# Performance work log

Measured on AMD Instinct MI355X. Metric: run time of the kernel, lower is better.

## Reference

```python
import jax, jax.numpy as jnp
import numpy as np

B, N, CQ, CH, H = 4, 1024, 512, 512, 8
D = CH // H  # head_dim = 64


def setup_inputs() -> dict:
    key = jax.random.key(0)
    ks = jax.random.split(key, 8)
    s = jnp.float32(0.02)  # realistic (non-degenerate) init scale instead of the module's zeros
    return {
        "q_x": jax.random.normal(ks[0], (B, N, CQ), jnp.float32),
        "attn_bias": jax.random.normal(ks[1], (B, H, N, N), jnp.float32),
        "Wq": jax.random.normal(ks[2], (CH, CQ), jnp.float32) * s,
        "bq": jnp.zeros((CH,), jnp.float32),
        "Wk": jax.random.normal(ks[3], (CH, CQ), jnp.float32) * s,  # LinearNoBias
        "Wv": jax.random.normal(ks[4], (CH, CQ), jnp.float32) * s,  # LinearNoBias
        "Wo": jax.random.normal(ks[5], (CQ, CH), jnp.float32) * s,
        "bo": jnp.zeros((CQ,), jnp.float32),
        "Wg": jax.random.normal(ks[6], (CQ, CQ), jnp.float32) * s,
        "bg": jnp.zeros((CQ,), jnp.float32),
        "gating_bias": jnp.ones((CQ,), jnp.float32),
    }


def reference(q_x, attn_bias, Wq, bq, Wk, Wv, Wo, bo, Wg, bg, gating_bias):
    Bq, Nq, _ = q_x.shape
    scale = jnp.asarray(D, q_x.dtype) ** -0.5
    # QKV projections; self-attention path (q_x is kv_x, ndim==3) applies scale to q
    q = (q_x @ Wq.T + bq).reshape(Bq, Nq, H, D).transpose(0, 2, 1, 3) * scale  # [B,H,N,D]
    k = (q_x @ Wk.T).reshape(Bq, Nq, H, D).transpose(0, 2, 1, 3)               # [B,H,N,D]
    v = (q_x @ Wv.T).reshape(Bq, Nq, H, D).transpose(0, 2, 1, 3)               # [B,H,N,D]
    # bias-augmented attention
    logits = jnp.einsum("bhqd,bhkd->bhqk", q, k) + attn_bias                    # [B,H,N,N]
    a = jax.nn.softmax(logits, axis=-1)
    o = jnp.einsum("bhqk,bhkd->bhqd", a, v)                                     # [B,H,N,D]
    o = o.transpose(0, 2, 1, 3).reshape(Bq, Nq, CH)                             # flatten heads
    out = o @ Wo.T + bo                                                         # to_out: c_hidden -> c_q
    # sigmoid gating with learned gating_bias (init ones)
    gate = jax.nn.sigmoid(q_x @ Wg.T + bg + gating_bias)
    return out * gate
```

## Files before the change

kernel.cpp:

```cpp
#include <hip/hip_runtime.h>
#include <math.h>


typedef __bf16 bf16x8 __attribute__((ext_vector_type(8)));
typedef float f32x4 __attribute__((ext_vector_type(4)));

__device__ __forceinline__ unsigned short f2bf(float f) {
    union { float f; unsigned u; } v; v.f = f;
    unsigned r = v.u + 0x7fff + ((v.u >> 16) & 1);
    return (unsigned short)(r >> 16);
}

__device__ __forceinline__ bf16x8 ldb8(const unsigned short* p) {
    union { float4 f; bf16x8 b; } u;
    u.f = *(const float4*)p;
    return u.b;
}

__global__ __launch_bounds__(256) void convert_kernel(
    const float* __restrict__ X, const float* __restrict__ Wq,
    const float* __restrict__ Wk, const float* __restrict__ Wg,
    const float* __restrict__ Wv, const float* __restrict__ Wo,
    unsigned short* __restrict__ Xb, unsigned short* __restrict__ Wcat)
{
    int i4 = (blockIdx.x * 256 + threadIdx.x) * 4;
    const float* src;
    unsigned short* dst;
    int off;
    if (i4 < 2097152) {
        src = X; dst = Xb; off = i4;
    } else {
        int g = i4 - 2097152;
        int sect = g >> 18;
        src = (sect == 0) ? Wq : (sect == 1) ? Wk : (sect == 2) ? Wg
            : (sect == 3) ? Wv : Wo;
        dst = Wcat + (sect << 18);
        off = g & 262143;
    }
    float4 v = *(const float4*)&src[off];
    ushort4 u;
    u.x = f2bf(v.x); u.y = f2bf(v.y); u.z = f2bf(v.z); u.w = f2bf(v.w);
    *(ushort4*)&dst[off] = u;
}

#define GSTR 40

__device__ __forceinline__ void gemm_core(
    const unsigned short* __restrict__ Ag,
    const unsigned short* __restrict__ Bg,
    unsigned short* __restrict__ Ab, unsigned short* __restrict__ Bb,
    f32x4 acc[4][4])
{
    const int tid = threadIdx.x;
    const int lane = tid & 63;
    const int quad = lane >> 4, lx = lane & 15;
    const int wid = tid >> 6;
    const int mw0 = (wid >> 1) * 64, nw0 = (wid & 1) * 64;
    const int rA = tid >> 2, cA = (tid & 3) * 8;
    const int l0 = rA * GSTR + cA;
    const int l1 = (rA + 64) * GSTR + cA;

    float4 a0 = *(const float4*)&Ag[(size_t)rA * 512 + cA];
    float4 a1 = *(const float4*)&Ag[(size_t)(rA + 64) * 512 + cA];
    float4 b0 = *(const float4*)&Bg[(size_t)rA * 512 + cA];
    float4 b1 = *(const float4*)&Bg[(size_t)(rA + 64) * 512 + cA];

#pragma unroll 1
    for (int k0 = 0; k0 < 512; k0 += 32) {
        *(float4*)&Ab[l0] = a0;
        *(float4*)&Ab[l1] = a1;
        *(float4*)&Bb[l0] = b0;
        *(float4*)&Bb[l1] = b1;
        __syncthreads();
        if (k0 < 480) {
            int kn = k0 + 32;
            a0 = *(const float4*)&Ag[(size_t)rA * 512 + kn + cA];
            a1 = *(const float4*)&Ag[(size_t)(rA + 64) * 512 + kn + cA];
            b0 = *(const float4*)&Bg[(size_t)rA * 512 + kn + cA];
            b1 = *(const float4*)&Bg[(size_t)(rA + 64) * 512 + kn + cA];
        }
        bf16x8 af[4], bfr[4];
#pragma unroll
        for (int mi = 0; mi < 4; ++mi)
            af[mi] = ldb8(&Ab[(mw0 + mi * 16 + lx) * GSTR + quad * 8]);
#pragma unroll
        for (int ni = 0; ni < 4; ++ni)
            bfr[ni] = ldb8(&Bb[(nw0 + ni * 16 + lx) * GSTR + quad * 8]);
#pragma unroll
        for (int mi = 0; mi < 4; ++mi)
#pragma unroll
            for (int ni = 0; ni < 4; ++ni)
                acc[mi][ni] = __builtin_amdgcn_mfma_f32_16x16x32_bf16(
                    af[mi], bfr[ni], acc[mi][ni], 0, 0, 0);
        __syncthreads();
    }
}

__global__ __launch_bounds__(256) void proj_gemm(
    const unsigned short* __restrict__ Xb, const unsigned short* __restrict__ Wcat,
    const float* __restrict__ bq, const float* __restrict__ bg,
    const float* __restrict__ gbias,
    unsigned short* __restrict__ qb, unsigned short* __restrict__ kb,
    unsigned short* __restrict__ vtb, float* __restrict__ gateb)
{
    __shared__ __align__(16) unsigned short Ab[128 * GSTR];
    __shared__ __align__(16) unsigned short Bb[128 * GSTR];
    const int row0 = blockIdx.x * 128;
    const int colv0 = blockIdx.y * 128;
    f32x4 acc[4][4];
#pragma unroll
    for (int i = 0; i < 4; ++i)
#pragma unroll
        for (int j = 0; j < 4; ++j) acc[i][j] = (f32x4){0.f, 0.f, 0.f, 0.f};

    gemm_core(Xb + (size_t)row0 * 512, Wcat + (size_t)colv0 * 512, Ab, Bb, acc);

    const int tid = threadIdx.x;
    const int lane = tid & 63;
    const int quad = lane >> 4, lx = lane & 15;
    const int wid = tid >> 6;
    const int mw0 = (wid >> 1) * 64, nw0 = (wid & 1) * 64;
    const int wsel = colv0 >> 9;
    const int ncb = colv0 & 511;

    if (wsel == 0) {
#pragma unroll
        for (int mi = 0; mi < 4; ++mi) {
#pragma unroll
            for (int ni = 0; ni < 4; ++ni) {
                int ch = ncb + nw0 + ni * 16 + lx;
                int h = ch >> 6, d = ch & 63;
                float bias = bq[ch];
#pragma unroll
                for (int r = 0; r < 4; ++r) {
                    int m = row0 + mw0 + mi * 16 + quad * 4 + r;
                    int b = m >> 10, nn = m & 1023;
                    qb[(size_t)(b * 8 + h) * 65536 + (size_t)nn * 64 + d] =
                        f2bf((acc[mi][ni][r] + bias) * 0.125f);
                }
            }
        }
    } else if (wsel == 1) {
#pragma unroll
        for (int mi = 0; mi < 4; ++mi) {
#pragma unroll
            for (int ni = 0; ni < 4; ++ni) {
                int ch = ncb + nw0 + ni * 16 + lx;
                int h = ch >> 6, d = ch & 63;
#pragma unroll
                for (int r = 0; r < 4; ++r) {
                    int m = row0 + mw0 + mi * 16 + quad * 4 + r;
                    int b = m >> 10, nn = m & 1023;
                    kb[(size_t)(b * 8 + h) * 65536 + (size_t)nn * 64 + d] =
                        f2bf(acc[mi][ni][r]);
                }
            }
        }
    } else if (wsel == 2) {
#pragma unroll
        for (int mi = 0; mi < 4; ++mi) {
#pragma unroll
            for (int ni = 0; ni < 4; ++ni) {
                int ch = ncb + nw0 + ni * 16 + lx;
                float bias = bg[ch] + gbias[ch];
#pragma unroll
                for (int r = 0; r < 4; ++r) {
                    int m = row0 + mw0 + mi * 16 + quad * 4 + r;
                    float z = acc[mi][ni][r] + bias;
                    gateb[(size_t)m * 512 + ch] = 1.f / (1.f + __expf(-z));
                }
            }
        }
    } else {
#pragma unroll
        for (int mi = 0; mi < 4; ++mi) {
            int tok0 = row0 + mw0 + mi * 16 + quad * 4;
            int b = tok0 >> 10, nn0 = tok0 & 1023;
#pragma unroll
            for (int ni = 0; ni < 4; ++ni) {
                int ch = ncb + nw0 + ni * 16 + lx;
                int h = ch >> 6, d = ch & 63;
                ushort4 u;
                u.x = f2bf(acc[mi][ni][0]);
                u.y = f2bf(acc[mi][ni][1]);
                u.z = f2bf(acc[mi][ni][2]);
                u.w = f2bf(acc[mi][ni][3]);
                *(ushort4*)&vtb[(size_t)(b * 8 + h) * 65536 + (size_t)d * 1024 + nn0] = u;
            }
        }
    }
}

#define LSTR 72

__global__ __launch_bounds__(256) void attn_kernel(
    const unsigned short* __restrict__ qb, const unsigned short* __restrict__ kb,
    const unsigned short* __restrict__ vtb, const float* __restrict__ bias,
    unsigned short* __restrict__ obb)
{
    __shared__ unsigned short QPs[64 * LSTR];
    __shared__ unsigned short Ks[64 * LSTR];
    __shared__ unsigned short Vt[64 * LSTR];

    const int tid = threadIdx.x;
    const int bh = blockIdx.y;
    const int qr0 = blockIdx.x * 64;
    const int wv = tid >> 6, lane = tid & 63;
    const int quad = lane >> 4, lx = lane & 15;
    const int qw0 = wv * 16;

    const unsigned short* qp = qb + (size_t)bh * 65536;
    const unsigned short* kp = kb + (size_t)bh * 65536;
    const unsigned short* vp = vtb + (size_t)bh * 65536;
    const float* bp = bias + (size_t)bh * 1048576;

    const int sr0 = tid >> 3, sc0 = (tid & 7) * 8;
    const int sr1 = (tid + 256) >> 3, sc1 = (tid & 7) * 8;

    *(float4*)&QPs[sr0 * LSTR + sc0] = *(const float4*)&qp[(size_t)(qr0 + sr0) * 64 + sc0];
    *(float4*)&QPs[sr1 * LSTR + sc1] = *(const float4*)&qp[(size_t)(qr0 + sr1) * 64 + sc1];

    float4 kr0 = *(const float4*)&kp[(size_t)sr0 * 64 + sc0];
    float4 kr1 = *(const float4*)&kp[(size_t)sr1 * 64 + sc1];
    float4 vr0 = *(const float4*)&vp[(size_t)sr0 * 1024 + sc0];
    float4 vr1 = *(const float4*)&vp[(size_t)sr1 * 1024 + sc1];

    const float* bbase = bp + (size_t)(qr0 + qw0 + quad * 4) * 1024 + lx;
    float bv[4][4];
#pragma unroll
    for (int r = 0; r < 4; ++r)
#pragma unroll
        for (int c = 0; c < 4; ++c)
            bv[r][c] = bbase[(size_t)r * 1024 + c * 16];

    __syncthreads();

    bf16x8 aq0 = ldb8(&QPs[(qw0 + lx) * LSTR + quad * 8]);
    bf16x8 aq1 = ldb8(&QPs[(qw0 + lx) * LSTR + 32 + quad * 8]);

    float l_i[4] = {0.f, 0.f, 0.f, 0.f};
    f32x4 oacc[4];
#pragma unroll
    for (int c = 0; c < 4; ++c) oacc[c] = (f32x4){0.f, 0.f, 0.f, 0.f};

#pragma unroll 1
    for (int kt = 0; kt < 16; ++kt) {
        __syncthreads();
        *(float4*)&Ks[sr0 * LSTR + sc0] = kr0;
        *(float4*)&Ks[sr1 * LSTR + sc1] = kr1;
        *(float4*)&Vt[sr0 * LSTR + sc0] = vr0;
        *(float4*)&Vt[sr1 * LSTR + sc1] = vr1;
        __syncthreads();

        const int ktn = (kt + 1) & 15;
        kr0 = *(const float4*)&kp[(size_t)(ktn * 64 + sr0) * 64 + sc0];
        kr1 = *(const float4*)&kp[(size_t)(ktn * 64 + sr1) * 64 + sc1];
        vr0 = *(const float4*)&vp[(size_t)sr0 * 1024 + ktn * 64 + sc0];
        vr1 = *(const float4*)&vp[(size_t)sr1 * 1024 + ktn * 64 + sc1];
        float bvn[4][4];
#pragma unroll
        for (int r = 0; r < 4; ++r)
#pragma unroll
            for (int c = 0; c < 4; ++c)
                bvn[r][c] = bbase[(size_t)r * 1024 + ktn * 64 + c * 16];

        f32x4 sacc[4];
#pragma unroll
        for (int c = 0; c < 4; ++c) {
            bf16x8 bk0 = ldb8(&Ks[(c * 16 + lx) * LSTR + quad * 8]);
            bf16x8 bk1 = ldb8(&Ks[(c * 16 + lx) * LSTR + 32 + quad * 8]);
            f32x4 z = {0.f, 0.f, 0.f, 0.f};
            z = __builtin_amdgcn_mfma_f32_16x16x32_bf16(aq0, bk0, z, 0, 0, 0);
            z = __builtin_amdgcn_mfma_f32_16x16x32_bf16(aq1, bk1, z, 0, 0, 0);
            sacc[c] = z;
        }

#pragma unroll
        for (int r = 0; r < 4; ++r) {
            float p0 = __expf(sacc[0][r] + bv[r][0]);
            float p1 = __expf(sacc[1][r] + bv[r][1]);
            float p2 = __expf(sacc[2][r] + bv[r][2]);
            float p3 = __expf(sacc[3][r] + bv[r][3]);
            l_i[r] += p0 + p1 + p2 + p3;
            int prow = (qw0 + quad * 4 + r) * LSTR;
            QPs[prow + 0 * 16 + lx] = f2bf(p0);
            QPs[prow + 1 * 16 + lx] = f2bf(p1);
            QPs[prow + 2 * 16 + lx] = f2bf(p2);
            QPs[prow + 3 * 16 + lx] = f2bf(p3);
        }

        bf16x8 ap0 = ldb8(&QPs[(qw0 + lx) * LSTR + quad * 8]);
        bf16x8 ap1 = ldb8(&QPs[(qw0 + lx) * LSTR + 32 + quad * 8]);
#pragma unroll
        for (int c = 0; c < 4; ++c) {
            bf16x8 bv0 = ldb8(&Vt[(c * 16 + lx) * LSTR + quad * 8]);
            bf16x8 bv1 = ldb8(&Vt[(c * 16 + lx) * LSTR + 32 + quad * 8]);
            oacc[c] = __builtin_amdgcn_mfma_f32_16x16x32_bf16(ap0, bv0, oacc[c], 0, 0, 0);
            oacc[c] = __builtin_amdgcn_mfma_f32_16x16x32_bf16(ap1, bv1, oacc[c], 0, 0, 0);
        }

#pragma unroll
        for (int r = 0; r < 4; ++r)
#pragma unroll
            for (int c = 0; c < 4; ++c)
                bv[r][c] = bvn[r][c];
    }

    const int b = bh >> 3, h = bh & 7;
#pragma unroll
    for (int r = 0; r < 4; ++r) {
        float lt = l_i[r];
        lt += __shfl_xor(lt, 1);
        lt += __shfl_xor(lt, 2);
        lt += __shfl_xor(lt, 4);
        lt += __shfl_xor(lt, 8);
        float inv = 1.f / lt;
        int row = qr0 + qw0 + quad * 4 + r;
        unsigned short* op = obb + (size_t)(b * 1024 + row) * 512 + h * 64 + lx;
#pragma unroll
        for (int c = 0; c < 4; ++c)
            op[c * 16] = f2bf(oacc[c][r] * inv);
    }
}

__global__ __launch_bounds__(256) void out_gemm(
    const unsigned short* __restrict__ A, const unsigned short* __restrict__ WoB,
    const float* __restrict__ bo, const float* __restrict__ gateb,
    float* __restrict__ out)
{
    __shared__ __align__(16) unsigned short Ab[64 * GSTR];
    __shared__ __align__(16) unsigned short Bb[128 * GSTR];
    const int tid = threadIdx.x;
    const int row0 = blockIdx.x * 64;
    const int n0 = blockIdx.y * 128;
    const unsigned short* Ag = A + (size_t)row0 * 512;
    const unsigned short* Bg = WoB + (size_t)n0 * 512;

    const int lane = tid & 63;
    const int quad = lane >> 4, lx = lane & 15;
    const int wid = tid >> 6;
    const int mw0 = (wid & 1) * 32, nw0 = (wid >> 1) * 64;
    const int rA = tid >> 2, cA = (tid & 3) * 8;
    const int lA = rA * GSTR + cA;
    const int lB0 = lA;
    const int lB1 = (rA + 64) * GSTR + cA;

    f32x4 acc[2][4];
#pragma unroll
    for (int i = 0; i < 2; ++i)
#pragma unroll
        for (int j = 0; j < 4; ++j) acc[i][j] = (f32x4){0.f, 0.f, 0.f, 0.f};

    float4 a0 = *(const float4*)&Ag[(size_t)rA * 512 + cA];
    float4 b0 = *(const float4*)&Bg[(size_t)rA * 512 + cA];
    float4 b1 = *(const float4*)&Bg[(size_t)(rA + 64) * 512 + cA];

#pragma unroll 1
    for (int k0 = 0; k0 < 512; k0 += 32) {
        *(float4*)&Ab[lA] = a0;
        *(float4*)&Bb[lB0] = b0;
        *(float4*)&Bb[lB1] = b1;
        __syncthreads();
        if (k0 < 480) {
            int kn = k0 + 32;
            a0 = *(const float4*)&Ag[(size_t)rA * 512 + kn + cA];
            b0 = *(const float4*)&Bg[(size_t)rA * 512 + kn + cA];
            b1 = *(const float4*)&Bg[(size_t)(rA + 64) * 512 + kn + cA];
        }
        bf16x8 af[2], bfr[4];
#pragma unroll
        for (int mi = 0; mi < 2; ++mi)
            af[mi] = ldb8(&Ab[(mw0 + mi * 16 + lx) * GSTR + quad * 8]);
#pragma unroll
        for (int ni = 0; ni < 4; ++ni)
            bfr[ni] = ldb8(&Bb[(nw0 + ni * 16 + lx) * GSTR + quad * 8]);
#pragma unroll
        for (int mi = 0; mi < 2; ++mi)
#pragma unroll
            for (int ni = 0; ni < 4; ++ni)
                acc[mi][ni] = __builtin_amdgcn_mfma_f32_16x16x32_bf16(
                    af[mi], bfr[ni], acc[mi][ni], 0, 0, 0);
        __syncthreads();
    }

#pragma unroll
    for (int mi = 0; mi < 2; ++mi) {
#pragma unroll
        for (int ni = 0; ni < 4; ++ni) {
            int n = n0 + nw0 + ni * 16 + lx;
            float bias = bo[n];
#pragma unroll
            for (int r = 0; r < 4; ++r) {
                int m = row0 + mw0 + mi * 16 + quad * 4 + r;
                out[(size_t)m * 512 + n] =
                    (acc[mi][ni][r] + bias) * gateb[(size_t)m * 512 + n];
            }
        }
    }
}

extern "C" void kernel_launch(void* const* d_in, const int* in_sizes, int n_in,
                              void* d_out, int out_size, void* d_ws, size_t ws_size,
                              hipStream_t stream) {
    (void)in_sizes; (void)n_in; (void)out_size; (void)ws_size;
    const float* q_x   = (const float*)d_in[0];
    const float* bias  = (const float*)d_in[1];
    const float* Wq    = (const float*)d_in[2];
    const float* bq    = (const float*)d_in[3];
    const float* Wk    = (const float*)d_in[4];
    const float* Wv    = (const float*)d_in[5];
    const float* Wo    = (const float*)d_in[6];
    const float* bo    = (const float*)d_in[7];
    const float* Wg    = (const float*)d_in[8];
    const float* bg    = (const float*)d_in[9];
    const float* gbias = (const float*)d_in[10];
    float* out = (float*)d_out;

    char* ws = (char*)d_ws;
    unsigned short* qb   = (unsigned short*)ws;
    unsigned short* kb   = (unsigned short*)(ws + (4u << 20));
    unsigned short* vtb  = (unsigned short*)(ws + (8u << 20));
    float* gateb         = (float*)(ws + (12u << 20));
    unsigned short* obb  = (unsigned short*)(ws + (20u << 20));
    unsigned short* Xb   = (unsigned short*)(ws + (24u << 20));
    unsigned short* Wcat = (unsigned short*)(ws + (28u << 20));

    convert_kernel<<<3328, 256, 0, stream>>>(q_x, Wq, Wk, Wg, Wv, Wo, Xb, Wcat);
    proj_gemm<<<dim3(32, 16), dim3(256), 0, stream>>>(
        Xb, Wcat, bq, bg, gbias, qb, kb, vtb, gateb);
    attn_kernel<<<dim3(16, 32), dim3(256), 0, stream>>>(qb, kb, vtb, bias, obb);
    out_gemm<<<dim3(64, 4), dim3(256), 0, stream>>>(
        obb, Wcat + (size_t)2048 * 512, bo, gateb, out);
}
```

Before: 266.2 us.

## Fuse all stages into one cooperative persistent kernel with grid syncs

Replaces the four separate launches (convert, projection GEMM, attention, output GEMM) with a single cooperative kernel of 512 blocks that runs each stage in turn, separated by grid-wide barriers. The aim is to remove per-launch overhead and inter-kernel gaps. The out-GEMM stage is re-tiled to 64x64 so it fits the fixed 512-block grid. The risks are grid-sync cost, occupancy limits from requesting two blocks per CU, and load imbalance because every stage is forced onto the same grid size. A fallback to the old multi-kernel path runs when occupancy is insufficient.

New measurement: 266.2 us. About the same (+0.0%).

```diff
diff --git a/kernel.cpp b/kernel.cpp
--- a/kernel.cpp
+++ b/kernel.cpp
@@ -1,5 +1,8 @@
 #include <hip/hip_runtime.h>
+#include <hip/hip_cooperative_groups.h>
 #include <math.h>
+
+namespace cg = cooperative_groups;
 
 
 typedef __bf16 bf16x8 __attribute__((ext_vector_type(8)));
@@ -15,6 +18,357 @@
     union { float4 f; bf16x8 b; } u;
     u.f = *(const float4*)p;
     return u.b;
+}
+
+#define GSTR 40
+#define LSTR 72
+
+__global__ __launch_bounds__(256, 2) void fused_kernel(
+    const float* __restrict__ X, const float* __restrict__ bias,
+    const float* __restrict__ Wq, const float* __restrict__ bq,
+    const float* __restrict__ Wk, const float* __restrict__ Wv,
+    const float* __restrict__ Wo, const float* __restrict__ bo,
+    const float* __restrict__ Wg, const float* __restrict__ bg,
+    const float* __restrict__ gbias, float* __restrict__ out,
+    unsigned short* __restrict__ qb, unsigned short* __restrict__ kb,
+    unsigned short* __restrict__ vtb, float* __restrict__ gateb,
+    unsigned short* __restrict__ obb,
+    unsigned short* __restrict__ Xb, unsigned short* __restrict__ Wcat)
+{
+    cg::grid_group grid = cg::this_grid();
+    __shared__ __align__(16) unsigned short smem[14336];
+
+    const int blk = blockIdx.x;
+    const int tid = threadIdx.x;
+    const int lane = tid & 63;
+    const int quad = lane >> 4, lx = lane & 15;
+    const int wid = tid >> 6;
+
+    {
+        int idx = blk * 256 + tid;
+#pragma unroll 1
+        for (int it = 0; it < 7; ++it) {
+            int chunk = idx + it * 131072;
+            if (chunk < 851968) {
+                int i4 = chunk * 4;
+                const float* src; unsigned short* dst; int off;
+                if (i4 < 2097152) { src = X; dst = Xb; off = i4; }
+                else {
+                    int g = i4 - 2097152;
+                    int sect = g >> 18;
+                    src = (sect == 0) ? Wq : (sect == 1) ? Wk : (sect == 2) ? Wg
+                        : (sect == 3) ? Wv : Wo;
+                    dst = Wcat + (sect << 18);
+                    off = g & 262143;
+                }
+                float4 v = *(const float4*)&src[off];
+                ushort4 u;
+                u.x = f2bf(v.x); u.y = f2bf(v.y); u.z = f2bf(v.z); u.w = f2bf(v.w);
+                *(ushort4*)&dst[off] = u;
+            }
+        }
+    }
+    grid.sync();
+
+    {
+        unsigned short* Ab = smem;
+        unsigned short* Bb = smem + 128 * GSTR;
+        const int row0 = (blk & 31) * 128;
+        const int colv0 = (blk >> 5) * 128;
+        const unsigned short* Ag = Xb + (size_t)row0 * 512;
+        const unsigned short* Bg = Wcat + (size_t)colv0 * 512;
+        const int mw0 = (wid >> 1) * 64, nw0 = (wid & 1) * 64;
+        const int rA = tid >> 2, cA = (tid & 3) * 8;
+        const int l0 = rA * GSTR + cA;
+        const int l1 = (rA + 64) * GSTR + cA;
+
+        f32x4 acc[4][4];
+#pragma unroll
+        for (int i = 0; i < 4; ++i)
+#pragma unroll
+            for (int j = 0; j < 4; ++j) acc[i][j] = (f32x4){0.f, 0.f, 0.f, 0.f};
+
+        float4 a0 = *(const float4*)&Ag[(size_t)rA * 512 + cA];
+        float4 a1 = *(const float4*)&Ag[(size_t)(rA + 64) * 512 + cA];
+        float4 b0 = *(const float4*)&Bg[(size_t)rA * 512 + cA];
+        float4 b1 = *(const float4*)&Bg[(size_t)(rA + 64) * 512 + cA];
+
+#pragma unroll 1
+        for (int k0 = 0; k0 < 512; k0 += 32) {
+            *(float4*)&Ab[l0] = a0;
+            *(float4*)&Ab[l1] = a1;
+            *(float4*)&Bb[l0] = b0;
+            *(float4*)&Bb[l1] = b1;
+            __syncthreads();
+            if (k0 < 480) {
+                int kn = k0 + 32;
+                a0 = *(const float4*)&Ag[(size_t)rA * 512 + kn + cA];
+                a1 = *(const float4*)&Ag[(size_t)(rA + 64) * 512 + kn + cA];
+                b0 = *(const float4*)&Bg[(size_t)rA * 512 + kn + cA];
+                b1 = *(const float4*)&Bg[(size_t)(rA + 64) * 512 + kn + cA];
+            }
+            bf16x8 af[4], bfr[4];
+#pragma unroll
+            for (int mi = 0; mi < 4; ++mi)
+                af[mi] = ldb8(&Ab[(mw0 + mi * 16 + lx) * GSTR + quad * 8]);
+#pragma unroll
+            for (int ni = 0; ni < 4; ++ni)
+                bfr[ni] = ldb8(&Bb[(nw0 + ni * 16 + lx) * GSTR + quad * 8]);
+#pragma unroll
+            for (int mi = 0; mi < 4; ++mi)
+#pragma unroll
+                for (int ni = 0; ni < 4; ++ni)
+                    acc[mi][ni] = __builtin_amdgcn_mfma_f32_16x16x32_bf16(
+                        af[mi], bfr[ni], acc[mi][ni], 0, 0, 0);
+            __syncthreads();
+        }
+
+        const int wsel = colv0 >> 9;
+        const int ncb = colv0 & 511;
+        if (wsel == 0) {
+#pragma unroll
+            for (int mi = 0; mi < 4; ++mi) {
+#pragma unroll
+                for (int ni = 0; ni < 4; ++ni) {
+                    int ch = ncb + nw0 + ni * 16 + lx;
+                    int h = ch >> 6, d = ch & 63;
+                    float bb = bq[ch];
+#pragma unroll
+                    for (int r = 0; r < 4; ++r) {
+                        int m = (blk & 31) * 128 + mw0 + mi * 16 + quad * 4 + r;
+                        int b = m >> 10, nn = m & 1023;
+                        qb[(size_t)(b * 8 + h) * 65536 + (size_t)nn * 64 + d] =
+                            f2bf((acc[mi][ni][r] + bb) * 0.125f);
+                    }
+                }
+            }
+        } else if (wsel == 1) {
+#pragma unroll
+            for (int mi = 0; mi < 4; ++mi) {
+#pragma unroll
+                for (int ni = 0; ni < 4; ++ni) {
+                    int ch = ncb + nw0 + ni * 16 + lx;
+                    int h = ch >> 6, d = ch & 63;
+#pragma unroll
+                    for (int r = 0; r < 4; ++r) {
+                        int m = (blk & 31) * 128 + mw0 + mi * 16 + quad * 4 + r;
+                        int b = m >> 10, nn = m & 1023;
+                        kb[(size_t)(b * 8 + h) * 65536 + (size_t)nn * 64 + d] =
+                            f2bf(acc[mi][ni][r]);
+                    }
+                }
+            }
+        } else if (wsel == 2) {
+#pragma unroll
+            for (int mi = 0; mi < 4; ++mi) {
+#pragma unroll
+                for (int ni = 0; ni < 4; ++ni) {
+                    int ch = ncb + nw0 + ni * 16 + lx;
+                    float bb = bg[ch] + gbias[ch];
+#pragma unroll
+                    for (int r = 0; r < 4; ++r) {
+                        int m = (blk & 31) * 128 + mw0 + mi * 16 + quad * 4 + r;
+                        float z = acc[mi][ni][r] + bb;
+                        gateb[(size_t)m * 512 + ch] = 1.f / (1.f + __expf(-z));
+                    }
+                }
+            }
+        } else {
+#pragma unroll
+            for (int mi = 0; mi < 4; ++mi) {
+                int tok0 = (blk & 31) * 128 + mw0 + mi * 16 + quad * 4;
+                int b = tok0 >> 10, nn0 = tok0 & 1023;
+#pragma unroll
+                for (int ni = 0; ni < 4; ++ni) {
+                    int ch = ncb + nw0 + ni * 16 + lx;
+                    int h = ch >> 6, d = ch & 63;
+                    ushort4 u;
+                    u.x = f2bf(acc[mi][ni][0]);
+                    u.y = f2bf(acc[mi][ni][1]);
+                    u.z = f2bf(acc[mi][ni][2]);
+                    u.w = f2bf(acc[mi][ni][3]);
+                    *(ushort4*)&vtb[(size_t)(b * 8 + h) * 65536 + (size_t)d * 1024 + nn0] = u;
+                }
+            }
+        }
+    }
+    grid.sync();
+
+    {
+        unsigned short* QPs = smem;
+        unsigned short* Ks  = smem + 64 * LSTR;
+        unsigned short* Vt  = smem + 128 * LSTR;
+        const int bh = blk >> 4;
+        const int qr0 = (blk & 15) * 64;
+        const int qw0 = wid * 16;
+
+        const unsigned short* qp = qb + (size_t)bh * 65536;
+        const unsigned short* kp = kb + (size_t)bh * 65536;
+        const unsigned short* vp = vtb + (size_t)bh * 65536;
+        const float* bp = bias + (size_t)bh * 1048576;
+
+        const int sr0 = tid >> 3, sc0 = (tid & 7) * 8;
+        const int sr1 = (tid + 256) >> 3, sc1 = (tid & 7) * 8;
+
+        *(float4*)&QPs[sr0 * LSTR + sc0] = *(const float4*)&qp[(size_t)(qr0 + sr0) * 64 + sc0];
+        *(float4*)&QPs[sr1 * LSTR + sc1] = *(const float4*)&qp[(size_t)(qr0 + sr1) * 64 + sc1];
+
+        float4 kr0 = *(const float4*)&kp[(size_t)sr0 * 64 + sc0];
+        float4 kr1 = *(const float4*)&kp[(size_t)sr1 * 64 + sc1];
+        float4 vr0 = *(const float4*)&vp[(size_t)sr0 * 1024 + sc0];
+        float4 vr1 = *(const float4*)&vp[(size_t)sr1 * 1024 + sc1];
+
+        const float* bbase = bp + (size_t)(qr0 + qw0 + quad * 4) * 1024 + lx;
+        float bv[4][4];
+#pragma unroll
+        for (int r = 0; r < 4; ++r)
+#pragma unroll
+            for (int c = 0; c < 4; ++c)
+                bv[r][c] = bbase[(size_t)r * 1024 + c * 16];
+
+        __syncthreads();
+
+        bf16x8 aq0 = ldb8(&QPs[(qw0 + lx) * LSTR + quad * 8]);
+        bf16x8 aq1 = ldb8(&QPs[(qw0 + lx) * LSTR + 32 + quad * 8]);
+
+        float l_i[4] = {0.f, 0.f, 0.f, 0.f};
+        f32x4 oacc[4];
+#pragma unroll
+        for (int c = 0; c < 4; ++c) oacc[c] = (f32x4){0.f, 0.f, 0.f, 0.f};
+
+#pragma unroll 1
+        for (int kt = 0; kt < 16; ++kt) {
+            __syncthreads();
+            *(float4*)&Ks[sr0 * LSTR + sc0] = kr0;
+            *(float4*)&Ks[sr1 * LSTR + sc1] = kr1;
+            *(float4*)&Vt[sr0 * LSTR + sc0] = vr0;
+            *(float4*)&Vt[sr1 * LSTR + sc1] = vr1;
+            __syncthreads();
+
+            const int ktn = (kt + 1) & 15;
+            kr0 = *(const float4*)&kp[(size_t)(ktn * 64 + sr0) * 64 + sc0];
+            kr1 = *(const float4*)&kp[(size_t)(ktn * 64 + sr1) * 64 + sc1];
+            vr0 = *(const float4*)&vp[(size_t)sr0 * 1024 + ktn * 64 + sc0];
+            vr1 = *(const float4*)&vp[(size_t)sr1 * 1024 + ktn * 64 + sc1];
+            float bvn[4][4];
+#pragma unroll
+            for (int r = 0; r < 4; ++r)
+#pragma unroll
+                for (int c = 0; c < 4; ++c)
+                    bvn[r][c] = bbase[(size_t)r * 1024 + ktn * 64 + c * 16];
+
+            f32x4 sacc[4];
+#pragma unroll
+            for (int c = 0; c < 4; ++c) {
+                bf16x8 bk0 = ldb8(&Ks[(c * 16 + lx) * LSTR + quad * 8]);
+                bf16x8 bk1 = ldb8(&Ks[(c * 16 + lx) * LSTR + 32 + quad * 8]);
+                f32x4 z = {0.f, 0.f, 0.f, 0.f};
+                z = __builtin_amdgcn_mfma_f32_16x16x32_bf16(aq0, bk0, z, 0, 0, 0);
+                z = __builtin_amdgcn_mfma_f32_16x16x32_bf16(aq1, bk1, z, 0, 0, 0);
+                sacc[c] = z;
+            }
+
+#pragma unroll
+            for (int r = 0; r < 4; ++r) {
+                float p0 = __expf(sacc[0][r] + bv[r][0]);
+                float p1 = __expf(sacc[1][r] + bv[r][1]);
+                float p2 = __expf(sacc[2][r] + bv[r][2]);
+                float p3 = __expf(sacc[3][r] + bv[r][3]);
+                l_i[r] += p0 + p1 + p2 + p3;
+                int prow = (qw0 + quad * 4 + r) * LSTR;
+                QPs[prow + 0 * 16 + lx] = f2bf(p0);
+                QPs[prow + 1 * 16 + lx] = f2bf(p1);
+                QPs[prow + 2 * 16 + lx] = f2bf(p2);
+                QPs[prow + 3 * 16 + lx] = f2bf(p3);
+            }
+
+            bf16x8 ap0 = ldb8(&QPs[(qw0 + lx) * LSTR + quad * 8]);
+            bf16x8 ap1 = ldb8(&QPs[(qw0 + lx) * LSTR + 32 + quad * 8]);
+#pragma unroll
+            for (int c = 0; c < 4; ++c) {
+                bf16x8 bv0 = ldb8(&Vt[(c * 16 + lx) * LSTR + quad * 8]);
+                bf16x8 bv1 = ldb8(&Vt[(c * 16 + lx) * LSTR + 32 + quad * 8]);
+                oacc[c] = __builtin_amdgcn_mfma_f32_16x16x32_bf16(ap0, bv0, oacc[c], 0, 0, 0);
+                oacc[c] = __builtin_amdgcn_mfma_f32_16x16x32_bf16(ap1, bv1, oacc[c], 0, 0, 0);
+            }
+
+#pragma unroll
+            for (int r = 0; r < 4; ++r)
+#pragma unroll
+                for (int c = 0; c < 4; ++c)
+                    bv[r][c] = bvn[r][c];
+        }
+
+        const int b = bh >> 3, h = bh & 7;
+#pragma unroll
+        for (int r = 0; r < 4; ++r) {
+            float lt = l_i[r];
+            lt += __shfl_xor(lt, 1);
+            lt += __shfl_xor(lt, 2);
+            lt += __shfl_xor(lt, 4);
+            lt += __shfl_xor(lt, 8);
+            float inv = 1.f / lt;
+            int row = qr0 + qw0 + quad * 4 + r;
+            unsigned short* op = obb + (size_t)(b * 1024 + row) * 512 + h * 64 + lx;
+#pragma unroll
+            for (int c = 0; c < 4; ++c)
+                op[c * 16] = f2bf(oacc[c][r] * inv);
+        }
+    }
+    grid.sync();
+
+    {
+        unsigned short* Ab = smem;
+        unsigned short* Bb = smem + 64 * GSTR;
+        const int row0 = (blk & 63) * 64;
+        const int n0 = (blk >> 6) * 64;
+        const unsigned short* Ag = obb + (size_t)row0 * 512;
+        const unsigned short* Bg = Wcat + (size_t)(2048 + n0) * 512;
+        const int mw = wid * 16;
+        const int rA = tid >> 2, cA = (tid & 3) * 8;
+        const int l0 = rA * GSTR + cA;
+
+        f32x4 acc[4];
+#pragma unroll
+        for (int j = 0; j < 4; ++j) acc[j] = (f32x4){0.f, 0.f, 0.f, 0.f};
+
+        float4 a0 = *(const float4*)&Ag[(size_t)rA * 512 + cA];
+        float4 b0 = *(const float4*)&Bg[(size_t)rA * 512 + cA];
+
+#pragma unroll 1
+        for (int k0 = 0; k0 < 512; k0 += 32) {
+            *(float4*)&Ab[l0] = a0;
+            *(float4*)&Bb[l0] = b0;
+            __syncthreads();
+            if (k0 < 480) {
+                int kn = k0 + 32;
+                a0 = *(const float4*)&Ag[(size_t)rA * 512 + kn + cA];
+                b0 = *(const float4*)&Bg[(size_t)rA * 512 + kn + cA];
+            }
+            bf16x8 af = ldb8(&Ab[(mw + lx) * GSTR + quad * 8]);
+            bf16x8 bfr[4];
+#pragma unroll
+            for (int ni = 0; ni < 4; ++ni)
+                bfr[ni] = ldb8(&Bb[(ni * 16 + lx) * GSTR + quad * 8]);
+#pragma unroll
+            for (int ni = 0; ni < 4; ++ni)
+                acc[ni] = __builtin_amdgcn_mfma_f32_16x16x32_bf16(
+                    af, bfr[ni], acc[ni], 0, 0, 0);
+            __syncthreads();
+        }
+
+#pragma unroll
+        for (int ni = 0; ni < 4; ++ni) {
+            int n = n0 + ni * 16 + lx;
+            float bb = bo[n];
+#pragma unroll
+            for (int r = 0; r < 4; ++r) {
+                int m = row0 + mw + quad * 4 + r;
+                out[(size_t)m * 512 + n] =
+                    (acc[ni][r] + bb) * gateb[(size_t)m * 512 + n];
+            }
+        }
+    }
 }
 
 __global__ __launch_bounds__(256) void convert_kernel(
@@ -43,11 +397,8 @@
     *(ushort4*)&dst[off] = u;
 }
 
-#define GSTR 40
-
 __device__ __forceinline__ void gemm_core(
-    const unsigned short* __restrict__ Ag,
-    const unsigned short* __restrict__ Bg,
+    const unsigned short* __restrict__ Ag, const unsigned short* __restrict__ Bg,
     unsigned short* __restrict__ Ab, unsigned short* __restrict__ Bb,
     f32x4 acc[4][4])
 {
@@ -125,24 +476,23 @@
 
     if (wsel == 0) {
 #pragma unroll
-        for (int mi = 0; mi < 4; ++mi) {
+        for (int mi = 0; mi < 4; ++mi)
 #pragma unroll
             for (int ni = 0; ni < 4; ++ni) {
                 int ch = ncb + nw0 + ni * 16 + lx;
                 int h = ch >> 6, d = ch & 63;
-                float bias = bq[ch];
+                float bb = bq[ch];
 #pragma unroll
                 for (int r = 0; r < 4; ++r) {
                     int m = row0 + mw0 + mi * 16 + quad * 4 + r;
                     int b = m >> 10, nn = m & 1023;
                     qb[(size_t)(b * 8 + h) * 65536 + (size_t)nn * 64 + d] =
-                        f2bf((acc[mi][ni][r] + bias) * 0.125f);
+                        f2bf((acc[mi][ni][r] + bb) * 0.125f);
                 }
             }
-        }
     } else if (wsel == 1) {
 #pragma unroll
-        for (int mi = 0; mi < 4; ++mi) {
+        for (int mi = 0; mi < 4; ++mi)
 #pragma unroll
             for (int ni = 0; ni < 4; ++ni) {
                 int ch = ncb + nw0 + ni * 16 + lx;
@@ -155,22 +505,20 @@
                         f2bf(acc[mi][ni][r]);
                 }
             }
-        }
     } else if (wsel == 2) {
 #pragma unroll
-        for (int mi = 0; mi < 4; ++mi) {
+        for (int mi = 0; mi < 4; ++mi)
 #pragma unroll
             for (int ni = 0; ni < 4; ++ni) {
                 int ch = ncb + nw0 + ni * 16 + lx;
-                float bias = bg[ch] + gbias[ch];
+                float bb = bg[ch] + gbias[ch];
 #pragma unroll
                 for (int r = 0; r < 4; ++r) {
                     int m = row0 + mw0 + mi * 16 + quad * 4 + r;
-                    float z = acc[mi][ni][r] + bias;
+                    float z = acc[mi][ni][r] + bb;
                     gateb[(size_t)m * 512 + ch] = 1.f / (1.f + __expf(-z));
                 }
             }
-        }
     } else {
 #pragma unroll
         for (int mi = 0; mi < 4; ++mi) {
@@ -190,8 +538,6 @@
         }
     }
 }
-
-#define LSTR 72
 
 __global__ __launch_bounds__(256) void attn_kernel(
     const unsigned short* __restrict__ qb, const unsigned short* __restrict__ kb,
@@ -342,7 +688,6 @@
     const int mw0 = (wid & 1) * 32, nw0 = (wid >> 1) * 64;
     const int rA = tid >> 2, cA = (tid & 3) * 8;
     const int lA = rA * GSTR + cA;
-    const int lB0 = lA;
     const int lB1 = (rA + 64) * GSTR + cA;
 
     f32x4 acc[2][4];
@@ -358,7 +703,7 @@
 #pragma unroll 1
     for (int k0 = 0; k0 < 512; k0 += 32) {
         *(float4*)&Ab[lA] = a0;
-        *(float4*)&Bb[lB0] = b0;
+        *(float4*)&Bb[lA] = b0;
         *(float4*)&Bb[lB1] = b1;
         __syncthreads();
         if (k0 < 480) {
@@ -384,19 +729,18 @@
     }
 
 #pragma unroll
-    for (int mi = 0; mi < 2; ++mi) {
+    for (int mi = 0; mi < 2; ++mi)
 #pragma unroll
         for (int ni = 0; ni < 4; ++ni) {
             int n = n0 + nw0 + ni * 16 + lx;
-            float bias = bo[n];
+            float bb = bo[n];
 #pragma unroll
             for (int r = 0; r < 4; ++r) {
                 int m = row0 + mw0 + mi * 16 + quad * 4 + r;
                 out[(size_t)m * 512 + n] =
-                    (acc[mi][ni][r] + bias) * gateb[(size_t)m * 512 + n];
-            }
-        }
-    }
+                    (acc[mi][ni][r] + bb) * gateb[(size_t)m * 512 + n];
+            }
+        }
 }
 
 extern "C" void kernel_launch(void* const* d_in, const int* in_sizes, int n_in,
@@ -425,10 +769,24 @@
     unsigned short* Xb   = (unsigned short*)(ws + (24u << 20));
     unsigned short* Wcat = (unsigned short*)(ws + (28u << 20));
 
-    convert_kernel<<<3328, 256, 0, stream>>>(q_x, Wq, Wk, Wg, Wv, Wo, Xb, Wcat);
-    proj_gemm<<<dim3(32, 16), dim3(256), 0, stream>>>(
-        Xb, Wcat, bq, bg, gbias, qb, kb, vtb, gateb);
-    attn_kernel<<<dim3(16, 32), dim3(256), 0, stream>>>(qb, kb, vtb, bias, obb);
-    out_gemm<<<dim3(64, 4), dim3(256), 0, stream>>>(
-        obb, Wcat + (size_t)2048 * 512, bo, gateb, out);
-}
+    int occ = 0;
+    hipError_t e = hipOccupancyMaxActiveBlocksPerMultiprocessor(
+        &occ, (const void*)fused_kernel, 256, 0);
+
+    if (e == hipSuccess && occ >= 2) {
+        void* args[] = {
+            (void*)&q_x, (void*)&bias, (void*)&Wq, (void*)&bq, (void*)&Wk,
+            (void*)&Wv, (void*)&Wo, (void*)&bo, (void*)&Wg, (void*)&bg,
+            (void*)&gbias, (void*)&out, (void*)&qb, (void*)&kb, (void*)&vtb,
+            (void*)&gateb, (void*)&obb, (void*)&Xb, (void*)&Wcat };
+        hipLaunchCooperativeKernel((const void*)fused_kernel,
+                                   dim3(512), dim3(256), args, 0, stream);
+    } else {
+        convert_kernel<<<3328, 256, 0, stream>>>(q_x, Wq, Wk, Wg, Wv, Wo, Xb, Wcat);
+        proj_gemm<<<dim3(32, 16), dim3(256), 0, stream>>>(
+            Xb, Wcat, bq, bg, gbias, qb, kb, vtb, gateb);
+        attn_kernel<<<dim3(16, 32), dim3(256), 0, stream>>>(qb, kb, vtb, bias, obb);
+        out_gemm<<<dim3(64, 4), dim3(256), 0, stream>>>(
+            obb, Wcat + (size_t)2048 * 512, bo, gateb, out);
+    }
+}
```
